# Kernel optimization log

Measured on AMD Instinct MI355X. Metric: run time of the kernel, lower is better.

Reference implementation:

```python
import jax, jax.numpy as jnp
import numpy as np

D = 4
R = 6
P = 2 * R + 1          # 13, fine match window
N = P * P              # 169
MR = 12
MP = 2 * MR + 1        # 25, coarse search window
DIL_INT = 15


def corr_sampler(t, r, Pp, dil):
    """SpatialCorrelationSampler(kernel_size=1, patch_size=Pp, dilation_patch=dil).
    t, r: (b,c,h,w). Returns (b,Pp,Pp,h,w): corr[b,p,q,y,x] = sum_c t[b,c,y,x]*r[b,c,y+dil*(p-R),x+dil*(q-R)] (zero pad)."""
    Rr = (Pp - 1) // 2
    pad = Rr * dil
    b, c, h, w = t.shape
    rp = jnp.pad(r, ((0, 0), (0, 0), (pad, pad), (pad, pad)))
    d = (jnp.arange(Pp) - Rr) * dil
    yi = jnp.arange(h)[None, :] + d[:, None] + pad      # (Pp,h)
    xi = jnp.arange(w)[None, :] + d[:, None] + pad      # (Pp,w)
    g = rp[:, :, yi[:, None, :, None], xi[None, :, None, :]]  # (b,c,Pp,Pp,h,w)
    return jnp.einsum('bchw,bcpqhw->bpqhw', t, g)


def bilinear_patch(src, py, px):
    """deform_im2col: bilinear-sample a PxP patch around (x+off_x+dx, y+off_y+dy).
    src (b,c,h,w); py (b,P,1,h,w); px (b,1,P,h,w) float coords. Returns (b,c,P,P,h,w)."""
    b, c, h, w = src.shape
    y0 = jnp.floor(py); x0 = jnp.floor(px)
    wy = py - y0; wx = px - x0
    y0 = y0.astype(jnp.int32); x0 = x0.astype(jnp.int32)

    def corner(yi, xi, wgt):
        valid = (yi >= 0) & (yi < h) & (xi >= 0) & (xi < w)
        yc = jnp.clip(yi, 0, h - 1)
        xc = jnp.clip(xi, 0, w - 1)
        v = jax.vmap(lambda im, a, bb: im[:, a, bb])(src, yc, xc)  # (b,c,P,P,h,w)
        return v * (wgt * valid)[:, None]

    out = corner(y0, x0, (1 - wy) * (1 - wx))
    out = out + corner(y0, x0 + 1, (1 - wy) * wx)
    out = out + corner(y0 + 1, x0, wy * (1 - wx))
    out = out + corner(y0 + 1, x0 + 1, wy * wx)
    return out


def unfold_patches(src, Pp):
    """F.unfold(src, kernel_size=Pp, padding=Rr) -> (b,c,Pp,Pp,h,w)."""
    Rr = (Pp - 1) // 2
    b, c, h, w = src.shape
    sp = jnp.pad(src, ((0, 0), (0, 0), (Rr, Rr), (Rr, Rr)))
    yi = jnp.arange(h)[None, :] + jnp.arange(Pp)[:, None]
    xi = jnp.arange(w)[None, :] + jnp.arange(Pp)[:, None]
    return sp[:, :, yi[:, None, :, None], xi[None, :, None, :]]


def _forward(feats_r, feats_t, quantized_r, nsearch, dirates):
    nref = feats_r.shape[0]
    b, c, h, w = feats_t.shape
    f32 = feats_t.dtype
    dy = (jnp.arange(P) - R).astype(f32)
    gy, gx = jnp.meshgrid(jnp.arange(-MR, MR + 1).astype(f32),
                          jnp.arange(-MR, MR + 1).astype(f32), indexing='ij')
    corrs = []
    py = px = None
    for si in range(nsearch):
        d = dirates[si]
        cc = corr_sampler(feats_t, feats_r[si], MP, d)                     # (b,MP,MP,h,w)
        cc = jax.nn.softmax(cc.reshape(b, MP * MP, h * w), axis=1).reshape(b, MP, MP, h, w)
        off_x = jnp.einsum('bpqhw,pq->bhw', cc, gx) * d                    # soft-argmax offsets
        off_y = jnp.einsum('bpqhw,pq->bhw', cc, gy) * d
        # sample coords: (b,P,1,h,w) / (b,1,P,h,w)
        py = (off_y + jnp.arange(h).astype(f32)[None, :, None])[:, None, None] + dy[:, None, None, None]
        px = (off_x + jnp.arange(w).astype(f32)[None, None, :])[:, None, None] + dy[None, :, None, None]
        col = bilinear_patch(feats_r[si], py, px)                          # (b,c,P,P,h,w)
        corrs.append(jnp.einsum('bchw,bcpqhw->bpqhw', feats_t, col).reshape(b, N, h * w))
    for ind in range(nsearch, nref):
        corrs.append(corr_sampler(feats_t, feats_r[ind], P, 1).reshape(b, N, h * w))
    corr = jax.nn.softmax(jnp.concatenate(corrs, 1), axis=1)               # (b,nref*N,hw)
    qr = quantized_r[:, :, :, ::D, ::D]                                    # prep(): (nref,b,C,h,w)
    cols = []
    for i in range(nsearch):
        # NOTE: faithful to original -- uses offset0 from the LAST coarse-search iteration
        cols.append(bilinear_patch(qr[i], py, px).reshape(b, -1, N, h * w))
    for i in range(nsearch, nref):
        cols.append(unfold_patches(qr[i], P).reshape(b, -1, N, h * w))
    image_uf = jnp.concatenate(cols, 2)                                    # (b,C,nref*N,hw)
    out = jnp.einsum('bnx,bcnx->bcx', corr, image_uf)
    return out.reshape(b, qr.shape[2], h, w)


def reference(feats_r, feats_t, quantized_r, ref_index, current_ind):
    gaps = [int(current_ind) - int(x) for x in np.asarray(ref_index)]
    nsearch = sum(g > DIL_INT for g in gaps)
    dirates = [min(4, g // DIL_INT + 1) for g in gaps if g > DIL_INT]
    return _forward(feats_r, feats_t, quantized_r, nsearch, dirates)


def setup_inputs():
    key = jax.random.key(0)
    k1, k2, k3 = jax.random.split(key, 3)
    feats_r = jax.random.normal(k1, (3, 1, 64, 48, 84), jnp.float32)
    feats_t = jax.random.normal(k2, (1, 64, 48, 84), jnp.float32)
    quantized_r = jax.random.uniform(k3, (3, 1, 32, 192, 336), jnp.float32)
    return dict(feats_r=feats_r, feats_t=feats_t, quantized_r=quantized_r,
                ref_index=np.arange(3), current_ind=16)
```

## Files before the change

### kernel.cpp

```cpp
#include <hip/hip_runtime.h>
#include <math.h>

constexpr int H  = 48;
constexpr int W  = 84;
constexpr int HW = H * W;
constexpr int C  = 64;
constexpr int CQ = 32;
constexpr int QH = 192;
constexpr int QW = 336;
constexpr int NREF = 3;
constexpr int SLG = 176;
constexpr int LGS = 544;

typedef short bf16x8 __attribute__((ext_vector_type(8)));
typedef float f32x4  __attribute__((ext_vector_type(4)));

#define DEV __device__ __forceinline__

DEV unsigned short f2bf_rn(float f) {
  unsigned int u = __builtin_bit_cast(unsigned int, f);
  u += 0x7FFFu + ((u >> 16) & 1u);
  return (unsigned short)(u >> 16);
}
DEV float bf2f(unsigned short h) {
  unsigned int u = ((unsigned int)h) << 16;
  return __builtin_bit_cast(float, u);
}

DEV float block_sum(float v, float* red) {
  __syncthreads();
#pragma unroll
  for (int o = 32; o > 0; o >>= 1) v += __shfl_down(v, o, 64);
  if ((threadIdx.x & 63) == 0) red[threadIdx.x >> 6] = v;
  __syncthreads();
  return red[0] + red[1] + red[2] + red[3];
}
DEV float block_max(float v, float* red) {
  __syncthreads();
#pragma unroll
  for (int o = 32; o > 0; o >>= 1) v = fmaxf(v, __shfl_down(v, o, 64));
  if ((threadIdx.x & 63) == 0) red[threadIdx.x >> 6] = v;
  __syncthreads();
  return fmaxf(fmaxf(red[0], red[1]), fmaxf(red[2], red[3]));
}

__global__ __launch_bounds__(256) void k_prep(const float* __restrict__ fr,
                                              const float* __restrict__ ft,
                                              const float* __restrict__ q,
                                              float* __restrict__ frT,
                                              float* __restrict__ ftT,
                                              unsigned short* __restrict__ rbh,
                                              unsigned short* __restrict__ rbl,
                                              unsigned short* __restrict__ tbh,
                                              unsigned short* __restrict__ tbl,
                                              unsigned short* __restrict__ qrb,
                                              float* __restrict__ accum) {
  __shared__ float lds[64][65];
  const int mode = blockIdx.y;
  const int tid = threadIdx.x;

  if (mode < 4) {
    const int r = mode;
    const float* src = (r < NREF) ? (fr + (size_t)r * C * HW) : ft;
    float* dstF          = (r < NREF) ? (frT + (size_t)r * HW * C) : ftT;
    unsigned short* dstH = (r < NREF) ? (rbh + (size_t)r * HW * C) : tbh;
    unsigned short* dstL = (r < NREF) ? (rbl + (size_t)r * HW * C) : tbl;
    const int pb = blockIdx.x * 64;
    const int a = tid & 63, b = tid >> 6;
#pragma unroll
    for (int i = 0; i < 16; i++) {
      int c = i * 4 + b;
      lds[c][a] = src[c * HW + pb + a];
    }
    __syncthreads();
#pragma unroll
    for (int i = 0; i < 16; i++) {
      int p = i * 4 + b;
      float v = lds[a][p];
      int o = (pb + p) * C + a;
      dstF[o] = v;
      unsigned short h = f2bf_rn(v);
      dstH[o] = h;
      dstL[o] = f2bf_rn(v - bf2f(h));
    }
  } else if (mode < 7) {
    const int k = mode - 4;
    const int yq = blockIdx.x;
    if (yq >= H) return;
    unsigned short* qs = (unsigned short*)lds;
    const int c = tid >> 3, xo = tid & 7;
#pragma unroll
    for (int i = 0; i < 11; i++) {
      const int x = xo + 8 * i;
      if (x < W) {
        const float v = q[((size_t)(k * CQ + c) * QH + yq * 4) * QW + x * 4];
        qs[x * CQ + c] = f2bf_rn(v);
      }
    }
    __syncthreads();
    const unsigned int* qsu = (const unsigned int*)qs;
    unsigned int* dst = (unsigned int*)(qrb + (size_t)k * HW * CQ + (size_t)yq * W * CQ);
    for (int o = tid; o < W * CQ / 2; o += 256) dst[o] = qsu[o];
  } else {
    const int nacc = NREF * HW * 3;
    for (int i = blockIdx.x * 256 + tid; i < nacc; i += 63 * 256) accum[i] = 0.f;
  }
}

DEV f32x4 band_mfma(bf16x8 ah0, bf16x8 ah1, bf16x8 al0, bf16x8 al1,
                    const unsigned short* __restrict__ rH,
                    const unsigned short* __restrict__ rL,
                    int bpix, int fko, bool bv) {
  const bf16x8 zf = {0, 0, 0, 0, 0, 0, 0, 0};
  bf16x8 bh0 = *reinterpret_cast<const bf16x8*>(rH + (size_t)bpix * C + fko);
  bf16x8 bh1 = *reinterpret_cast<const bf16x8*>(rH + (size_t)bpix * C + fko + 32);
  bf16x8 bl0 = *reinterpret_cast<const bf16x8*>(rL + (size_t)bpix * C + fko);
  bf16x8 bl1 = *reinterpret_cast<const bf16x8*>(rL + (size_t)bpix * C + fko + 32);
  if (!bv) { bh0 = zf; bh1 = zf; bl0 = zf; bl1 = zf; }
  f32x4 acc = {0.f, 0.f, 0.f, 0.f};
  acc = __builtin_amdgcn_mfma_f32_16x16x32_bf16(ah0, bh0, acc, 0, 0, 0);
  acc = __builtin_amdgcn_mfma_f32_16x16x32_bf16(ah1, bh1, acc, 0, 0, 0);
  acc = __builtin_amdgcn_mfma_f32_16x16x32_bf16(ah0, bl0, acc, 0, 0, 0);
  acc = __builtin_amdgcn_mfma_f32_16x16x32_bf16(ah1, bl1, acc, 0, 0, 0);
  acc = __builtin_amdgcn_mfma_f32_16x16x32_bf16(al0, bh0, acc, 0, 0, 0);
  acc = __builtin_amdgcn_mfma_f32_16x16x32_bf16(al1, bh1, acc, 0, 0, 0);
  return acc;
}

__global__ __launch_bounds__(256) void k_mfma(
    const unsigned short* __restrict__ rbh, const unsigned short* __restrict__ rbl,
    const unsigned short* __restrict__ tbh, const unsigned short* __restrict__ tbl,
    const int* __restrict__ ridx, const int* __restrict__ curp,
    float* __restrict__ accum, float* __restrict__ lg) {
  const int bid = blockIdx.x;
  const int idx = bid >> 3;
  const int ychunk = bid & 7;
  const int yloc = idx / 72;
  const int rest = idx - yloc * 72;
  const int zi = rest / 6;
  const int x0i = rest - zi * 6;
  const int y = ychunk * 6 + yloc;
  const int x0 = x0i * 16;
  const int si = zi >> 2, pz = zi & 3;

  const int gap = curp[0] - ridx[si];
  const bool isSearch = gap > 15;
  const int lane = threadIdx.x & 63, wave = threadIdx.x >> 6;
  if (!isSearch && pz >= 2) return;

  const int fpx = lane & 15, fko = (lane >> 4) * 8;
  const bool pValid = (x0 + fpx) < W;
  const int apix = pValid ? (y * W + x0 + fpx) : 0;
  const bf16x8 zf = {0, 0, 0, 0, 0, 0, 0, 0};
  bf16x8 ah0 = *reinterpret_cast<const bf16x8*>(tbh + (size_t)apix * C + fko);
  bf16x8 ah1 = *reinterpret_cast<const bf16x8*>(tbh + (size_t)apix * C + fko + 32);
  bf16x8 al0 = *reinterpret_cast<const bf16x8*>(tbl + (size_t)apix * C + fko);
  bf16x8 al1 = *reinterpret_cast<const bf16x8*>(tbl + (size_t)apix * C + fko + 32);
  if (!pValid) { ah0 = zf; ah1 = zf; al0 = zf; al1 = zf; }

  const unsigned short* rH = rbh + (size_t)si * HW * C;
  const unsigned short* rL = rbl + (size_t)si * HW * C;

  if (isSearch) {
    int d = gap / 15 + 1; if (d > 4) d = 4;
    const int Zoff = (d == 1) ? 16 : (d == 2) ? 32 : 48;
    const int NZT  = (d == 1) ? 3  : (d == 2) ? 5  : 7;
    const int Minv = (d == 1) ? 65536 : (d == 2) ? 32768 : (d == 3) ? 21846 : 16384;
    const int slot = pz * 4 + wave;
    const int p1 = slot, p2 = slot + 16;
    const float w2 = (p2 <= 24) ? 1.f : 0.f;
    const int row2a = y + d * (p1 - 12);
    const int row2b = y + d * (p2 - 12);
    const bool rva = (row2a >= 0) && (row2a < H);
    const bool rvb = (w2 > 0.f) && (row2b >= 0) && (row2b < H);

    float seA[4] = {0.f, 0.f, 0.f, 0.f};
    float seB[4] = {0.f, 0.f, 0.f, 0.f};
    float sq[4]  = {0.f, 0.f, 0.f, 0.f};

    for (int zt = 0; zt < NZT; ++zt) {
      const int z0 = x0 - Zoff + zt * 16;
      const int z = z0 + fpx;
      const bool zv = (z >= 0) && (z < W);
      const bool bva = rva && zv, bvb = rvb && zv;
      const int bpa = bva ? (row2a * W + z) : 0;
      const int bpb = bvb ? (row2b * W + z) : 0;
      f32x4 accA = band_mfma(ah0, ah1, al0, al1, rH, rL, bpa, fko, bva);
      f32x4 accB = band_mfma(ah0, ah1, al0, al1, rH, rL, bpb, fko, bvb);
#pragma unroll
      for (int r = 0; r < 4; r++) {
        const int xl = (lane >> 4) * 4 + r;
        const int qnum = (z0 + fpx) - (x0 + xl) + 12 * d;
        if (qnum >= 0) {
          const int qq = (qnum * Minv) >> 16;
          if (qq * d == qnum && qq < 25) {
            const float eA = __expf(fminf(accA[r], 60.f));
            const float eB = w2 * __expf(fminf(accB[r], 60.f));
            seA[r] += eA; seB[r] += eB;
            sq[r] += (eA + eB) * (float)(qq - 12);
          }
        }
      }
    }
#pragma unroll
    for (int r = 0; r < 4; r++) {
#pragma unroll
      for (int o = 1; o < 16; o <<= 1) {
        seA[r] += __shfl_xor(seA[r], o, 64);
        seB[r] += __shfl_xor(seB[r], o, 64);
        sq[r]  += __shfl_xor(sq[r],  o, 64);
      }
    }
    if (fpx == 0) {
#pragma unroll
      for (int r = 0; r < 4; r++) {
        const int xl = (lane >> 4) * 4 + r;
        if (x0 + xl < W) {
          float* a = accum + (size_t)(si * HW + y * W + x0 + xl) * 3;
          atomicAdd(a + 0, seA[r] + seB[r]);
          atomicAdd(a + 1, seA[r] * (float)(p1 - 12) + seB[r] * (float)(p2 - 12));
          atomicAdd(a + 2, sq[r]);
        }
      }
    }
  } else {
    const int slot = pz * 4 + wave;
    const int dp1 = slot, dp2 = slot + 8;
    const bool has2 = dp2 < 13;
    const int row2a = y + dp1 - 6;
    const int row2b = y + dp2 - 6;
    const bool rva = (row2a >= 0) && (row2a < H);
    const bool rvb = has2 && (row2b >= 0) && (row2b < H);

    for (int zt = 0; zt < 3; ++zt) {
      const int z0 = x0 - 16 + zt * 16;
      const int z = z0 + fpx;
      const bool zv = (z >= 0) && (z < W);
      const bool bva = rva && zv, bvb = rvb && zv;
      const int bpa = bva ? (row2a * W + z) : 0;
      const int bpb = bvb ? (row2b * W + z) : 0;
      f32x4 accA = band_mfma(ah0, ah1, al0, al1, rH, rL, bpa, fko, bva);
      f32x4 accB = band_mfma(ah0, ah1, al0, al1, rH, rL, bpb, fko, bvb);
#pragma unroll
      for (int r = 0; r < 4; r++) {
        const int xl = (lane >> 4) * 4 + r;
        const int qq = (z0 + fpx) - (x0 + xl) + 6;
        if (qq >= 0 && qq < 13 && (x0 + xl) < W) {
          float* lb = lg + (size_t)(y * W + x0 + xl) * LGS + si * SLG;
          lb[dp1 * 13 + qq] = accA[r];
          if (has2) lb[dp2 * 13 + qq] = accB[r];
        }
      }
    }
  }
}

__global__ __launch_bounds__(256) void k_pix(
    const float* __restrict__ frT, const float* __restrict__ ftT,
    const unsigned short* __restrict__ qrb, const float* __restrict__ lg,
    const float* __restrict__ accum,
    const int* __restrict__ ridx, const int* __restrict__ curp,
    float* __restrict__ out) {
  const int pix = blockIdx.x;
  const int y = pix / W, x = pix - y * W;
  const int tid = threadIdx.x;
  const int lane = tid & 63, wave = tid >> 6;

  __shared__ __align__(16) float tl[64];
  __shared__ float C14[14][16];
  __shared__ float sP[4];
  __shared__ float sLs[4];
  __shared__ __align__(16) float lgs[3 * SLG];
  __shared__ float red[4];
  __shared__ int   wloc[640];
  __shared__ float wval[640];
  __shared__ float part[4][32];

  const int cur = curp[0];
  bool srch[NREF];
  int dd[NREF];
  int ls = -1;
#pragma unroll
  for (int k = 0; k < NREF; k++) {
    const int g = cur - ridx[k];
    srch[k] = (g > 15);
    int d = g / 15 + 1;
    dd[k] = d > 4 ? 4 : d;
    if (srch[k]) ls = k;
  }

  if (tid < 64) tl[tid] = ftT[(size_t)pix * C + tid];
  if (tid < 21) lgs[(tid / 7) * SLG + 169 + (tid % 7)] = -1e30f;
  __syncthreads();

  for (int si = 0; si < NREF; ++si) {
    if (!srch[si]) continue;
    if (tid == 0) {
      const float* a = accum + (size_t)(si * HW + pix) * 3;
      const float inv = 1.f / a[0];
      const float oy = (float)dd[si] * a[1] * inv, ox = (float)dd[si] * a[2] * inv;
      const float fy = (float)y + oy, fx = (float)x + ox;
      const float Y0 = floorf(fy), X0 = floorf(fx);
      sP[0] = Y0; sP[1] = X0; sP[2] = fy - Y0; sP[3] = fx - X0;
      if (si == ls) { sLs[0] = Y0; sLs[1] = X0; sLs[2] = fy - Y0; sLs[3] = fx - X0; }
    }
    __syncthreads();
    const int iY = (int)sP[0], iX = (int)sP[1];
    const float wy = sP[2], wx = sP[3];
    const float* frB = frT + (size_t)si * HW * C;

    if (tid < 224) {
      const int j = tid >> 4, cg = tid & 15;
      const int col = iX - 6 + j;
      const bool cv = (col >= 0) && (col < W);
      const float4 tv = *reinterpret_cast<const float4*>(&tl[cg * 4]);
#pragma unroll 2
      for (int i = 0; i < 14; ++i) {
        const int row = iY - 6 + i;
        float s = 0.f;
        if (cv && row >= 0 && row < H) {
          const float4 rv4 = *reinterpret_cast<const float4*>(
              frB + (size_t)(row * W + col) * C + cg * 4);
          s = tv.x * rv4.x + tv.y * rv4.y + tv.z * rv4.z + tv.w * rv4.w;
        }
        s += __shfl_xor(s, 1, 64);
        s += __shfl_xor(s, 2, 64);
        s += __shfl_xor(s, 4, 64);
        s += __shfl_xor(s, 8, 64);
        if (cg == 0) C14[i][j] = s;
      }
    }
    __syncthreads();
    for (int it = tid; it < 169; it += 256) {
      const int i = it / 13, j = it - i * 13;
      lgs[si * SLG + it] =
          (1.f - wy) * ((1.f - wx) * C14[i][j] + wx * C14[i][j + 1]) +
          wy * ((1.f - wx) * C14[i + 1][j] + wx * C14[i + 1][j + 1]);
    }
    __syncthreads();
  }

  for (int k = 0; k < NREF; k++) {
    if (srch[k]) continue;
    const float* src = lg + (size_t)pix * LGS + k * SLG;
    for (int it = tid; it < 42; it += 256)
      *reinterpret_cast<float4*>(&lgs[k * SLG + it * 4]) =
          *reinterpret_cast<const float4*>(src + it * 4);
    if (tid == 42 * 4 - 168)
      lgs[k * SLG + 168] = src[168];
  }
  __syncthreads();

  float m = -1e30f;
  for (int i = tid; i < 3 * SLG; i += 256) m = fmaxf(m, lgs[i]);
  m = block_max(m, red);
  float se = 0.f;
  for (int i = tid; i < 3 * SLG; i += 256) {
    const float e = __expf(lgs[i] - m);
    lgs[i] = e;
    se += e;
  }
  se = block_sum(se, red);
  const float inv = 1.f / se;

  int bases[NREF], tot = 0;
#pragma unroll
  for (int k = 0; k < NREF; k++) { bases[k] = tot; tot += srch[k] ? 196 : 169; }
  const int NT = (tot + 63) >> 6;

  int liY = 0, liX = 0; float lwy = 0.f, lwx = 0.f;
  if (ls >= 0) { liY = (int)sLs[0]; liX = (int)sLs[1]; lwy = sLs[2]; lwx = sLs[3]; }

  for (int k = 0; k < NREF; k++) {
    const int base = bases[k];
    if (srch[k]) {
      const float* wk = &lgs[k * SLG];
      for (int it = tid; it < 196; it += 256) {
        const int i = it / 14, j = it - i * 14;
        const float a00 = (i < 13 && j < 13) ? wk[i * 13 + j] : 0.f;
        const float a01 = (i < 13 && j >= 1) ? wk[i * 13 + j - 1] : 0.f;
        const float a10 = (i >= 1 && j < 13) ? wk[(i - 1) * 13 + j] : 0.f;
        const float a11 = (i >= 1 && j >= 1) ? wk[(i - 1) * 13 + j - 1] : 0.f;
        const float wv = (1.f - lwy) * ((1.f - lwx) * a00 + lwx * a01) +
                         lwy * ((1.f - lwx) * a10 + lwx * a11);
        const int row = liY + i - 6, col = liX + j - 6;
        const bool v = (unsigned)row < (unsigned)H && (unsigned)col < (unsigned)W;
        wloc[base + it] = v ? (k * HW + row * W + col) : 0;
        wval[base + it] = v ? wv : 0.f;
      }
    } else {
      for (int it = tid; it < 169; it += 256) {
        const int p = it / 13, q = it - p * 13;
        const int row = y + p - 6, col = x + q - 6;
        const bool v = (unsigned)row < (unsigned)H && (unsigned)col < (unsigned)W;
        wloc[base + it] = v ? (k * HW + row * W + col) : 0;
        wval[base + it] = v ? lgs[k * SLG + it] : 0.f;
      }
    }
  }
  for (int e = tot + tid; e < NT * 64; e += 256) { wloc[e] = 0; wval[e] = 0.f; }
  __syncthreads();

  const int c4 = lane & 3, l16 = lane >> 2;
  float a[8] = {0.f, 0.f, 0.f, 0.f, 0.f, 0.f, 0.f, 0.f};
  for (int t = 0; t < NT; ++t) {
    const int e = t * 64 + wave * 16 + l16;
    const float wv = wval[e];
    const int loc = wloc[e];
    const bf16x8 qv = *reinterpret_cast<const bf16x8*>(
        qrb + (size_t)loc * CQ + c4 * 8);
#pragma unroll
    for (int j = 0; j < 8; j++)
      a[j] = fmaf(wv, bf2f((unsigned short)qv[j]), a[j]);
  }
#pragma unroll
  for (int o = 4; o < 64; o <<= 1) {
#pragma unroll
    for (int j = 0; j < 8; j++) a[j] += __shfl_xor(a[j], o, 64);
  }
  if (l16 == 0) {
#pragma unroll
    for (int j = 0; j < 8; j++) part[wave][c4 * 8 + j] = a[j];
  }
  __syncthreads();
  if (tid < 32) {
    const float s = part[0][tid] + part[1][tid] + part[2][tid] + part[3][tid];
    out[(size_t)tid * HW + pix] = s * inv;
  }
}

extern "C" void kernel_launch(void* const* d_in, const int* in_sizes, int n_in,
                              void* d_out, int out_size, void* d_ws, size_t ws_size,
                              hipStream_t stream) {
  (void)in_sizes; (void)n_in; (void)out_size; (void)ws_size;
  const float* fr = (const float*)d_in[0];
  const float* ft = (const float*)d_in[1];
  const float* q  = (const float*)d_in[2];
  const int* ridx = (const int*)d_in[3];
  const int* cur  = (const int*)d_in[4];
  float* out = (float*)d_out;

  char* ws = (char*)d_ws;
  float* frT  = (float*)ws;                   ws += (size_t)NREF * HW * C * 4;
  float* ftT  = (float*)ws;                   ws += (size_t)HW * C * 4;
  unsigned short* rbh = (unsigned short*)ws;  ws += (size_t)NREF * HW * C * 2;
  unsigned short* rbl = (unsigned short*)ws;  ws += (size_t)NREF * HW * C * 2;
  unsigned short* tbh = (unsigned short*)ws;  ws += (size_t)HW * C * 2;
  unsigned short* tbl = (unsigned short*)ws;  ws += (size_t)HW * C * 2;
  unsigned short* qrb = (unsigned short*)ws;  ws += (size_t)NREF * HW * CQ * 2;
  float* lg    = (float*)ws;                  ws += (size_t)HW * LGS * 4;
  float* accum = (float*)ws;                  ws += (size_t)NREF * HW * 3 * 4;

  k_prep<<<dim3(HW / 64, 8), dim3(256), 0, stream>>>(fr, ft, q, frT, ftT,
                                                     rbh, rbl, tbh, tbl, qrb, accum);
  k_mfma<<<dim3(8 * 432), dim3(256), 0, stream>>>(rbh, rbl, tbh, tbl,
                                                  ridx, cur, accum, lg);
  k_pix<<<dim3(HW), dim3(256), 0, stream>>>(frT, ftT, qrb, lg, accum,
                                            ridx, cur, out);
}
```

Baseline: 86.96 us.

## Store raw coarse-search logits and compute the softmax offset in the pixel kernel

The MFMA kernel no longer computes exp-sums with atomics for the coarse search. It writes the full 625 raw correlation logits per pixel to a new buffer, and the pixel kernel then does the max-subtracted softmax and offset reduction per block. Other changes: hi and lo bf16 planes are merged into one buffer with a zero sentinel row instead of predicated zeroing, B-operand loads are software-prefetched one tile ahead, the search and non-search paths are unified under a 3D grid, and the 14-row correlation loop is unrolled with the shuffle reductions batched. This removes the atomics and the accumulator zeroing, and makes the softmax stable. In exchange it writes and reads an extra buffer of about 3*HW*640 floats.

```diff
diff --git a/kernel.cpp b/kernel.cpp
--- a/kernel.cpp
+++ b/kernel.cpp
@@ -11,6 +11,13 @@
 constexpr int NREF = 3;
 constexpr int SLG = 176;
 constexpr int LGS = 544;
+constexpr int S625 = 640;
+
+constexpr int RROWS = NREF * HW;
+constexpr int RZERO = RROWS;
+constexpr int RLO   = RROWS + 1;
+constexpr int TZERO = HW;
+constexpr int TLO   = HW + 1;
 
 typedef short bf16x8 __attribute__((ext_vector_type(8)));
 typedef float f32x4  __attribute__((ext_vector_type(4)));
@@ -49,12 +56,9 @@
                                               const float* __restrict__ q,
                                               float* __restrict__ frT,
                                               float* __restrict__ ftT,
-                                              unsigned short* __restrict__ rbh,
-                                              unsigned short* __restrict__ rbl,
-                                              unsigned short* __restrict__ tbh,
-                                              unsigned short* __restrict__ tbl,
-                                              unsigned short* __restrict__ qrb,
-                                              float* __restrict__ accum) {
+                                              unsigned short* __restrict__ rb,
+                                              unsigned short* __restrict__ tb,
+                                              unsigned short* __restrict__ qrb) {
   __shared__ float lds[64][65];
   const int mode = blockIdx.y;
   const int tid = threadIdx.x;
@@ -63,8 +67,8 @@
     const int r = mode;
     const float* src = (r < NREF) ? (fr + (size_t)r * C * HW) : ft;
     float* dstF          = (r < NREF) ? (frT + (size_t)r * HW * C) : ftT;
-    unsigned short* dstH = (r < NREF) ? (rbh + (size_t)r * HW * C) : tbh;
-    unsigned short* dstL = (r < NREF) ? (rbl + (size_t)r * HW * C) : tbl;
+    unsigned short* dstH = (r < NREF) ? (rb + (size_t)r * HW * C) : tb;
+    const size_t loOff   = (size_t)((r < NREF) ? RLO : TLO) * C;
     const int pb = blockIdx.x * 64;
     const int a = tid & 63, b = tid >> 6;
 #pragma unroll
@@ -77,13 +81,19 @@
     for (int i = 0; i < 16; i++) {
       int p = i * 4 + b;
       float v = lds[a][p];
-      int o = (pb + p) * C + a;
+      size_t o = (size_t)(pb + p) * C + a;
       dstF[o] = v;
       unsigned short h = f2bf_rn(v);
       dstH[o] = h;
-      dstL[o] = f2bf_rn(v - bf2f(h));
-    }
-  } else if (mode < 7) {
+      dstH[o + loOff] = f2bf_rn(v - bf2f(h));
+    }
+    if (mode == 3 && blockIdx.x == 0 && tid < 64) {
+      rb[(size_t)RZERO * C + tid] = 0;
+      rb[(size_t)(RLO + RROWS) * C + tid] = 0;
+      tb[(size_t)TZERO * C + tid] = 0;
+      tb[(size_t)(TLO + HW) * C + tid] = 0;
+    }
+  } else {
     const int k = mode - 4;
     const int yq = blockIdx.x;
     if (yq >= H) return;
@@ -101,155 +111,89 @@
     const unsigned int* qsu = (const unsigned int*)qs;
     unsigned int* dst = (unsigned int*)(qrb + (size_t)k * HW * CQ + (size_t)yq * W * CQ);
     for (int o = tid; o < W * CQ / 2; o += 256) dst[o] = qsu[o];
-  } else {
-    const int nacc = NREF * HW * 3;
-    for (int i = blockIdx.x * 256 + tid; i < nacc; i += 63 * 256) accum[i] = 0.f;
-  }
-}
-
-DEV f32x4 band_mfma(bf16x8 ah0, bf16x8 ah1, bf16x8 al0, bf16x8 al1,
-                    const unsigned short* __restrict__ rH,
-                    const unsigned short* __restrict__ rL,
-                    int bpix, int fko, bool bv) {
-  const bf16x8 zf = {0, 0, 0, 0, 0, 0, 0, 0};
-  bf16x8 bh0 = *reinterpret_cast<const bf16x8*>(rH + (size_t)bpix * C + fko);
-  bf16x8 bh1 = *reinterpret_cast<const bf16x8*>(rH + (size_t)bpix * C + fko + 32);
-  bf16x8 bl0 = *reinterpret_cast<const bf16x8*>(rL + (size_t)bpix * C + fko);
-  bf16x8 bl1 = *reinterpret_cast<const bf16x8*>(rL + (size_t)bpix * C + fko + 32);
-  if (!bv) { bh0 = zf; bh1 = zf; bl0 = zf; bl1 = zf; }
-  f32x4 acc = {0.f, 0.f, 0.f, 0.f};
-  acc = __builtin_amdgcn_mfma_f32_16x16x32_bf16(ah0, bh0, acc, 0, 0, 0);
-  acc = __builtin_amdgcn_mfma_f32_16x16x32_bf16(ah1, bh1, acc, 0, 0, 0);
-  acc = __builtin_amdgcn_mfma_f32_16x16x32_bf16(ah0, bl0, acc, 0, 0, 0);
-  acc = __builtin_amdgcn_mfma_f32_16x16x32_bf16(ah1, bl1, acc, 0, 0, 0);
-  acc = __builtin_amdgcn_mfma_f32_16x16x32_bf16(al0, bh0, acc, 0, 0, 0);
-  acc = __builtin_amdgcn_mfma_f32_16x16x32_bf16(al1, bh1, acc, 0, 0, 0);
-  return acc;
+  }
 }
 
 __global__ __launch_bounds__(256) void k_mfma(
-    const unsigned short* __restrict__ rbh, const unsigned short* __restrict__ rbl,
-    const unsigned short* __restrict__ tbh, const unsigned short* __restrict__ tbl,
+    const unsigned short* __restrict__ rb, const unsigned short* __restrict__ tb,
     const int* __restrict__ ridx, const int* __restrict__ curp,
-    float* __restrict__ accum, float* __restrict__ lg) {
-  const int bid = blockIdx.x;
-  const int idx = bid >> 3;
-  const int ychunk = bid & 7;
-  const int yloc = idx / 72;
-  const int rest = idx - yloc * 72;
-  const int zi = rest / 6;
-  const int x0i = rest - zi * 6;
-  const int y = ychunk * 6 + yloc;
-  const int x0 = x0i * 16;
-  const int si = zi >> 2, pz = zi & 3;
-
+    float* __restrict__ lg, float* __restrict__ lg625) {
+  const int si = blockIdx.z / 7, pz = blockIdx.z % 7;
   const int gap = curp[0] - ridx[si];
   const bool isSearch = gap > 15;
   const int lane = threadIdx.x & 63, wave = threadIdx.x >> 6;
-  if (!isSearch && pz >= 2) return;
-
+  const int sub = pz * 4 + wave;
+  if (isSearch ? (sub >= 25) : (sub >= 13)) return;
+
+  const int y = blockIdx.y, x0 = blockIdx.x * 16;
   const int fpx = lane & 15, fko = (lane >> 4) * 8;
-  const bool pValid = (x0 + fpx) < W;
-  const int apix = pValid ? (y * W + x0 + fpx) : 0;
-  const bf16x8 zf = {0, 0, 0, 0, 0, 0, 0, 0};
-  bf16x8 ah0 = *reinterpret_cast<const bf16x8*>(tbh + (size_t)apix * C + fko);
-  bf16x8 ah1 = *reinterpret_cast<const bf16x8*>(tbh + (size_t)apix * C + fko + 32);
-  bf16x8 al0 = *reinterpret_cast<const bf16x8*>(tbl + (size_t)apix * C + fko);
-  bf16x8 al1 = *reinterpret_cast<const bf16x8*>(tbl + (size_t)apix * C + fko + 32);
-  if (!pValid) { ah0 = zf; ah1 = zf; al0 = zf; al1 = zf; }
-
-  const unsigned short* rH = rbh + (size_t)si * HW * C;
-  const unsigned short* rL = rbl + (size_t)si * HW * C;
-
+
+  const int gapix = (x0 + fpx < W) ? (y * W + x0 + fpx) : TZERO;
+  const unsigned short* tbb = tb + (size_t)gapix * C + fko;
+  const bf16x8 ah0 = *reinterpret_cast<const bf16x8*>(tbb);
+  const bf16x8 ah1 = *reinterpret_cast<const bf16x8*>(tbb + 32);
+  const bf16x8 al0 = *reinterpret_cast<const bf16x8*>(tbb + (size_t)TLO * C);
+  const bf16x8 al1 = *reinterpret_cast<const bf16x8*>(tbb + (size_t)TLO * C + 32);
+
+  int d = 1, Zoff = 16, NZT = 3, Minv = 65536, qoff = 6, qmax = 13;
   if (isSearch) {
-    int d = gap / 15 + 1; if (d > 4) d = 4;
-    const int Zoff = (d == 1) ? 16 : (d == 2) ? 32 : 48;
-    const int NZT  = (d == 1) ? 3  : (d == 2) ? 5  : 7;
-    const int Minv = (d == 1) ? 65536 : (d == 2) ? 32768 : (d == 3) ? 21846 : 16384;
-    const int slot = pz * 4 + wave;
-    const int p1 = slot, p2 = slot + 16;
-    const float w2 = (p2 <= 24) ? 1.f : 0.f;
-    const int row2a = y + d * (p1 - 12);
-    const int row2b = y + d * (p2 - 12);
-    const bool rva = (row2a >= 0) && (row2a < H);
-    const bool rvb = (w2 > 0.f) && (row2b >= 0) && (row2b < H);
-
-    float seA[4] = {0.f, 0.f, 0.f, 0.f};
-    float seB[4] = {0.f, 0.f, 0.f, 0.f};
-    float sq[4]  = {0.f, 0.f, 0.f, 0.f};
-
-    for (int zt = 0; zt < NZT; ++zt) {
-      const int z0 = x0 - Zoff + zt * 16;
-      const int z = z0 + fpx;
-      const bool zv = (z >= 0) && (z < W);
-      const bool bva = rva && zv, bvb = rvb && zv;
-      const int bpa = bva ? (row2a * W + z) : 0;
-      const int bpb = bvb ? (row2b * W + z) : 0;
-      f32x4 accA = band_mfma(ah0, ah1, al0, al1, rH, rL, bpa, fko, bva);
-      f32x4 accB = band_mfma(ah0, ah1, al0, al1, rH, rL, bpb, fko, bvb);
-#pragma unroll
-      for (int r = 0; r < 4; r++) {
-        const int xl = (lane >> 4) * 4 + r;
-        const int qnum = (z0 + fpx) - (x0 + xl) + 12 * d;
-        if (qnum >= 0) {
-          const int qq = (qnum * Minv) >> 16;
-          if (qq * d == qnum && qq < 25) {
-            const float eA = __expf(fminf(accA[r], 60.f));
-            const float eB = w2 * __expf(fminf(accB[r], 60.f));
-            seA[r] += eA; seB[r] += eB;
-            sq[r] += (eA + eB) * (float)(qq - 12);
-          }
-        }
-      }
-    }
+    d = gap / 15 + 1; if (d > 4) d = 4;
+    Zoff = (d == 1) ? 16 : (d == 2) ? 32 : 48;
+    NZT  = (d == 1) ? 3  : (d == 2) ? 5  : 7;
+    Minv = (d == 1) ? 65536 : (d == 2) ? 32768 : (d == 3) ? 21846 : 16384;
+    qoff = 12 * d; qmax = 25;
+  }
+  const int row2 = isSearch ? (y + d * (sub - 12)) : (y + sub - 6);
+  const bool rv = (row2 >= 0) && (row2 < H);
+  const int rowoff = si * HW + row2 * W;
+
+  float* sb[4];
+#pragma unroll
+  for (int r = 0; r < 4; r++) {
+    const int xl = (lane >> 4) * 4 + r;
+    sb[r] = isSearch
+        ? (lg625 + ((size_t)si * HW + y * W + x0 + xl) * S625 + sub * 25)
+        : (lg + (size_t)(y * W + x0 + xl) * LGS + si * SLG + sub * 13);
+  }
+
+  auto gofs = [&](int zt) -> size_t {
+    const int z = x0 - Zoff + zt * 16 + fpx;
+    const bool v = rv && (z >= 0) && (z < W);
+    const int gp = v ? (rowoff + z) : RZERO;
+    return (size_t)gp * C + fko;
+  };
+
+  size_t o = gofs(0);
+  bf16x8 nh0 = *reinterpret_cast<const bf16x8*>(rb + o);
+  bf16x8 nh1 = *reinterpret_cast<const bf16x8*>(rb + o + 32);
+  bf16x8 nl0 = *reinterpret_cast<const bf16x8*>(rb + o + (size_t)RLO * C);
+  bf16x8 nl1 = *reinterpret_cast<const bf16x8*>(rb + o + (size_t)RLO * C + 32);
+
+  for (int zt = 0; zt < NZT; ++zt) {
+    const bf16x8 bh0 = nh0, bh1 = nh1, bl0 = nl0, bl1 = nl1;
+    if (zt + 1 < NZT) {
+      o = gofs(zt + 1);
+      nh0 = *reinterpret_cast<const bf16x8*>(rb + o);
+      nh1 = *reinterpret_cast<const bf16x8*>(rb + o + 32);
+      nl0 = *reinterpret_cast<const bf16x8*>(rb + o + (size_t)RLO * C);
+      nl1 = *reinterpret_cast<const bf16x8*>(rb + o + (size_t)RLO * C + 32);
+    }
+    f32x4 acc = {0.f, 0.f, 0.f, 0.f};
+    acc = __builtin_amdgcn_mfma_f32_16x16x32_bf16(ah0, bh0, acc, 0, 0, 0);
+    acc = __builtin_amdgcn_mfma_f32_16x16x32_bf16(ah1, bh1, acc, 0, 0, 0);
+    acc = __builtin_amdgcn_mfma_f32_16x16x32_bf16(ah0, bl0, acc, 0, 0, 0);
+    acc = __builtin_amdgcn_mfma_f32_16x16x32_bf16(ah1, bl1, acc, 0, 0, 0);
+    acc = __builtin_amdgcn_mfma_f32_16x16x32_bf16(al0, bh0, acc, 0, 0, 0);
+    acc = __builtin_amdgcn_mfma_f32_16x16x32_bf16(al1, bh1, acc, 0, 0, 0);
+
+    const int zbase = x0 - Zoff + zt * 16 + fpx - x0 + qoff;
 #pragma unroll
     for (int r = 0; r < 4; r++) {
-#pragma unroll
-      for (int o = 1; o < 16; o <<= 1) {
-        seA[r] += __shfl_xor(seA[r], o, 64);
-        seB[r] += __shfl_xor(seB[r], o, 64);
-        sq[r]  += __shfl_xor(sq[r],  o, 64);
-      }
-    }
-    if (fpx == 0) {
-#pragma unroll
-      for (int r = 0; r < 4; r++) {
-        const int xl = (lane >> 4) * 4 + r;
-        if (x0 + xl < W) {
-          float* a = accum + (size_t)(si * HW + y * W + x0 + xl) * 3;
-          atomicAdd(a + 0, seA[r] + seB[r]);
-          atomicAdd(a + 1, seA[r] * (float)(p1 - 12) + seB[r] * (float)(p2 - 12));
-          atomicAdd(a + 2, sq[r]);
-        }
-      }
-    }
-  } else {
-    const int slot = pz * 4 + wave;
-    const int dp1 = slot, dp2 = slot + 8;
-    const bool has2 = dp2 < 13;
-    const int row2a = y + dp1 - 6;
-    const int row2b = y + dp2 - 6;
-    const bool rva = (row2a >= 0) && (row2a < H);
-    const bool rvb = has2 && (row2b >= 0) && (row2b < H);
-
-    for (int zt = 0; zt < 3; ++zt) {
-      const int z0 = x0 - 16 + zt * 16;
-      const int z = z0 + fpx;
-      const bool zv = (z >= 0) && (z < W);
-      const bool bva = rva && zv, bvb = rvb && zv;
-      const int bpa = bva ? (row2a * W + z) : 0;
-      const int bpb = bvb ? (row2b * W + z) : 0;
-      f32x4 accA = band_mfma(ah0, ah1, al0, al1, rH, rL, bpa, fko, bva);
-      f32x4 accB = band_mfma(ah0, ah1, al0, al1, rH, rL, bpb, fko, bvb);
-#pragma unroll
-      for (int r = 0; r < 4; r++) {
-        const int xl = (lane >> 4) * 4 + r;
-        const int qq = (z0 + fpx) - (x0 + xl) + 6;
-        if (qq >= 0 && qq < 13 && (x0 + xl) < W) {
-          float* lb = lg + (size_t)(y * W + x0 + xl) * LGS + si * SLG;
-          lb[dp1 * 13 + qq] = accA[r];
-          if (has2) lb[dp2 * 13 + qq] = accB[r];
-        }
+      const int xl = (lane >> 4) * 4 + r;
+      const int qnum = zbase - xl;
+      if (qnum >= 0) {
+        const int qq = (qnum * Minv) >> 16;
+        if (qq * d == qnum && qq < qmax && (x0 + xl) < W) sb[r][qq] = acc[r];
       }
     }
   }
@@ -258,7 +202,7 @@
 __global__ __launch_bounds__(256) void k_pix(
     const float* __restrict__ frT, const float* __restrict__ ftT,
     const unsigned short* __restrict__ qrb, const float* __restrict__ lg,
-    const float* __restrict__ accum,
+    const float* __restrict__ lg625,
     const int* __restrict__ ridx, const int* __restrict__ curp,
     float* __restrict__ out) {
   const int pix = blockIdx.x;
@@ -271,6 +215,7 @@
   __shared__ float sP[4];
   __shared__ float sLs[4];
   __shared__ __align__(16) float lgs[3 * SLG];
+  __shared__ __align__(16) float ls6[S625];
   __shared__ float red[4];
   __shared__ int   wloc[640];
   __shared__ float wval[640];
@@ -291,14 +236,33 @@
 
   if (tid < 64) tl[tid] = ftT[(size_t)pix * C + tid];
   if (tid < 21) lgs[(tid / 7) * SLG + 169 + (tid % 7)] = -1e30f;
-  __syncthreads();
 
   for (int si = 0; si < NREF; ++si) {
     if (!srch[si]) continue;
+    const float* Lp = lg625 + ((size_t)si * HW + pix) * S625;
+    __syncthreads();
+    if (tid < 156)
+      *reinterpret_cast<float4*>(&ls6[tid * 4]) =
+          *reinterpret_cast<const float4*>(Lp + tid * 4);
+    else if (tid == 156) ls6[624] = Lp[624];
+    else if (tid < 172) ls6[624 + tid - 156] = -1e30f;
+
+    float m = -1e30f;
+    for (int i = tid; i < S625; i += 256) m = fmaxf(m, ls6[i]);
+    m = block_max(m, red);
+    float se = 0.f, sy = 0.f, sx = 0.f;
+    for (int i = tid; i < S625; i += 256) {
+      const float e = __expf(ls6[i] - m);
+      const int p = (i * 5243) >> 17;
+      const int q = i - p * 25;
+      se += e; sy += e * (float)(p - 12); sx += e * (float)(q - 12);
+    }
+    se = block_sum(se, red);
+    sy = block_sum(sy, red);
+    sx = block_sum(sx, red);
     if (tid == 0) {
-      const float* a = accum + (size_t)(si * HW + pix) * 3;
-      const float inv = 1.f / a[0];
-      const float oy = (float)dd[si] * a[1] * inv, ox = (float)dd[si] * a[2] * inv;
+      const float inv = 1.f / se;
+      const float oy = (float)dd[si] * sy * inv, ox = (float)dd[si] * sx * inv;
       const float fy = (float)y + oy, fx = (float)x + ox;
       const float Y0 = floorf(fy), X0 = floorf(fx);
       sP[0] = Y0; sP[1] = X0; sP[2] = fy - Y0; sP[3] = fx - X0;
@@ -314,20 +278,27 @@
       const int col = iX - 6 + j;
       const bool cv = (col >= 0) && (col < W);
       const float4 tv = *reinterpret_cast<const float4*>(&tl[cg * 4]);
-#pragma unroll 2
+      float s[14];
+#pragma unroll
       for (int i = 0; i < 14; ++i) {
         const int row = iY - 6 + i;
-        float s = 0.f;
+        s[i] = 0.f;
         if (cv && row >= 0 && row < H) {
           const float4 rv4 = *reinterpret_cast<const float4*>(
               frB + (size_t)(row * W + col) * C + cg * 4);
-          s = tv.x * rv4.x + tv.y * rv4.y + tv.z * rv4.z + tv.w * rv4.w;
+          s[i] = tv.x * rv4.x + tv.y * rv4.y + tv.z * rv4.z + tv.w * rv4.w;
         }
-        s += __shfl_xor(s, 1, 64);
-        s += __shfl_xor(s, 2, 64);
-        s += __shfl_xor(s, 4, 64);
-        s += __shfl_xor(s, 8, 64);
-        if (cg == 0) C14[i][j] = s;
+      }
+#pragma unroll
+      for (int i = 0; i < 14; ++i) {
+        s[i] += __shfl_xor(s[i], 1, 64);
+        s[i] += __shfl_xor(s[i], 2, 64);
+        s[i] += __shfl_xor(s[i], 4, 64);
+        s[i] += __shfl_xor(s[i], 8, 64);
+      }
+      if (cg == 0) {
+#pragma unroll
+        for (int i = 0; i < 14; ++i) C14[i][j] = s[i];
       }
     }
     __syncthreads();
@@ -337,7 +308,6 @@
           (1.f - wy) * ((1.f - wx) * C14[i][j] + wx * C14[i][j + 1]) +
           wy * ((1.f - wx) * C14[i + 1][j] + wx * C14[i + 1][j + 1]);
     }
-    __syncthreads();
   }
 
   for (int k = 0; k < NREF; k++) {
@@ -346,8 +316,7 @@
     for (int it = tid; it < 42; it += 256)
       *reinterpret_cast<float4*>(&lgs[k * SLG + it * 4]) =
           *reinterpret_cast<const float4*>(src + it * 4);
-    if (tid == 42 * 4 - 168)
-      lgs[k * SLG + 168] = src[168];
+    if (tid == 42) lgs[k * SLG + 168] = src[168];
   }
   __syncthreads();
 
@@ -441,20 +410,18 @@
   float* out = (float*)d_out;
 
   char* ws = (char*)d_ws;
-  float* frT  = (float*)ws;                   ws += (size_t)NREF * HW * C * 4;
-  float* ftT  = (float*)ws;                   ws += (size_t)HW * C * 4;
-  unsigned short* rbh = (unsigned short*)ws;  ws += (size_t)NREF * HW * C * 2;
-  unsigned short* rbl = (unsigned short*)ws;  ws += (size_t)NREF * HW * C * 2;
-  unsigned short* tbh = (unsigned short*)ws;  ws += (size_t)HW * C * 2;
-  unsigned short* tbl = (unsigned short*)ws;  ws += (size_t)HW * C * 2;
-  unsigned short* qrb = (unsigned short*)ws;  ws += (size_t)NREF * HW * CQ * 2;
-  float* lg    = (float*)ws;                  ws += (size_t)HW * LGS * 4;
-  float* accum = (float*)ws;                  ws += (size_t)NREF * HW * 3 * 4;
-
-  k_prep<<<dim3(HW / 64, 8), dim3(256), 0, stream>>>(fr, ft, q, frT, ftT,
-                                                     rbh, rbl, tbh, tbl, qrb, accum);
-  k_mfma<<<dim3(8 * 432), dim3(256), 0, stream>>>(rbh, rbl, tbh, tbl,
-                                                  ridx, cur, accum, lg);
-  k_pix<<<dim3(HW), dim3(256), 0, stream>>>(frT, ftT, qrb, lg, accum,
+  float* frT  = (float*)ws;                  ws += (size_t)NREF * HW * C * 4;
+  float* ftT  = (float*)ws;                  ws += (size_t)HW * C * 4;
+  unsigned short* rb = (unsigned short*)ws;  ws += (size_t)2 * (NREF * HW + 1) * C * 2;
+  unsigned short* tb = (unsigned short*)ws;  ws += (size_t)2 * (HW + 1) * C * 2;
+  unsigned short* qrb = (unsigned short*)ws; ws += (size_t)NREF * HW * CQ * 2;
+  float* lg    = (float*)ws;                 ws += (size_t)HW * LGS * 4;
+  float* lg625 = (float*)ws;                 ws += (size_t)NREF * HW * S625 * 4;
+
+  k_prep<<<dim3(HW / 64, 7), dim3(256), 0, stream>>>(fr, ft, q, frT, ftT,
+                                                     rb, tb, qrb);
+  k_mfma<<<dim3(6, H, NREF * 7), dim3(256), 0, stream>>>(rb, tb, ridx, cur,
+                                                         lg, lg625);
+  k_pix<<<dim3(HW), dim3(256), 0, stream>>>(frT, ftT, qrb, lg, lg625,
                                             ridx, cur, out);
 }
```

Result: faster. 80.96 us (-6.9%).
